# Performance work log

Hardware: AMD Instinct MI355X
Metric: run time of the kernel (lower is better)

## Reference

```python
import jax, jax.numpy as jnp
import numpy as np

EPS = 1e-8

def elu_feature_map(x):
    return jax.nn.elu(x) + 1.0

def setup_inputs() -> dict:
    key = jax.random.key(0)
    ks = jax.random.split(key, 5)
    B, S, D = 2, 4096, 1024
    scale = 1.0 / np.sqrt(D).astype(np.float32)
    x = jax.random.normal(ks[0], (B, S, D), dtype=jnp.float32)
    Wq = jax.random.normal(ks[1], (D, D), dtype=jnp.float32) * scale
    Wk = jax.random.normal(ks[2], (D, D), dtype=jnp.float32) * scale
    Wv = jax.random.normal(ks[3], (D, D), dtype=jnp.float32) * scale
    Wo = jax.random.normal(ks[4], (D, D), dtype=jnp.float32) * scale
    return {"x": x, "Wq": Wq, "Wk": Wk, "Wv": Wv, "Wo": Wo}

def reference(x, Wq, Wk, Wv, Wo):
    B, S, D = x.shape
    H = 16
    Dh = D // H
    # projections (nn.Linear with no bias: x @ W.T)
    def proj(W):
        return (x @ W.T).reshape(B, S, H, Dh)
    q = elu_feature_map(proj(Wq))  # [B,S,H,Dh]
    k = elu_feature_map(proj(Wk))
    v = proj(Wv)
    # scan over sequence: carry running kv_sum [B,H,Dh,Dh] and k_sum [B,H,Dh]
    q_t = jnp.moveaxis(q, 1, 0)  # [S,B,H,Dh]
    k_t = jnp.moveaxis(k, 1, 0)
    v_t = jnp.moveaxis(v, 1, 0)

    def step(carry, qkv):
        kv_sum, k_sum = carry
        q_i, k_i, v_i = qkv  # each [B,H,Dh]
        kv_sum = kv_sum + jnp.einsum('bhd,bhe->bhde', k_i, v_i)
        k_sum = k_sum + k_i
        num = jnp.einsum('bhd,bhde->bhe', q_i, kv_sum)
        den = jnp.sum(q_i * k_sum, axis=-1, keepdims=True)
        out_i = num / (den + EPS)
        return (kv_sum, k_sum), out_i

    kv0 = jnp.zeros((B, H, Dh, Dh), dtype=x.dtype)
    ks0 = jnp.zeros((B, H, Dh), dtype=x.dtype)
    _, out = jax.lax.scan(step, (kv0, ks0), (q_t, k_t, v_t))  # out: [S,B,H,Dh]
    out = jnp.moveaxis(out, 0, 1).reshape(B, S, D)
    return out @ Wo.T
```

## Files before the change

### kernel.cpp

```cpp
#include <hip/hip_runtime.h>
#include <math.h>


#define EPSF 1e-8f

typedef unsigned short u16;
typedef unsigned int   u32;
typedef __attribute__((ext_vector_type(8))) short short8v;
typedef __attribute__((ext_vector_type(4))) float f32x4;

__device__ __forceinline__ float elu1(float x){ return x > 0.f ? x + 1.f : __expf(x); }
__device__ __forceinline__ u16 f2bf(float f){
    union{float f; u32 i;} c; c.f = f;
    u32 i = c.i + 0x7FFFu + ((c.i >> 16) & 1u);
    return (u16)(i >> 16);
}
__device__ __forceinline__ float bflo(u32 v){ union{u32 i; float f;} c; c.i = v << 16; return c.f; }
__device__ __forceinline__ float bfhi(u32 v){ union{u32 i; float f;} c; c.i = v & 0xffff0000u; return c.f; }
__device__ __forceinline__ void f4a(float4 v, float* a){ a[0]=v.x; a[1]=v.y; a[2]=v.z; a[3]=v.w; }

__device__ __forceinline__ void gload16(const void* g, void* l){
    __builtin_amdgcn_global_load_lds((const __attribute__((address_space(1))) u32*)g,
                                     (__attribute__((address_space(3))) u32*)l, 16, 0, 0);
}

__global__ __launch_bounds__(256) void k_cast5(
    const float* __restrict__ x,  const float* __restrict__ wq,
    const float* __restrict__ wk, const float* __restrict__ wv,
    const float* __restrict__ wo,
    u16* __restrict__ xb, u16* __restrict__ wcat, u16* __restrict__ wob)
{
    size_t i8 = ((size_t)blockIdx.x * 256 + threadIdx.x) * 8;
    const float* s; u16* d; size_t off;
    if      (i8 <  8388608) { s = x;  d = xb;            off = i8; }
    else if (i8 <  9437184) { s = wq; d = wcat;          off = i8 - 8388608; }
    else if (i8 < 10485760) { s = wk; d = wcat + 1048576; off = i8 - 9437184; }
    else if (i8 < 11534336) { s = wv; d = wcat + 2097152; off = i8 - 10485760; }
    else                    { s = wo; d = wob;           off = i8 - 11534336; }
    float4 a = *(const float4*)&s[off];
    float4 b = *(const float4*)&s[off + 4];
    uint4 p;
    p.x = (u32)f2bf(a.x) | ((u32)f2bf(a.y) << 16);
    p.y = (u32)f2bf(a.z) | ((u32)f2bf(a.w) << 16);
    p.z = (u32)f2bf(b.x) | ((u32)f2bf(b.y) << 16);
    p.w = (u32)f2bf(b.z) | ((u32)f2bf(b.w) << 16);
    *(uint4*)&d[off] = p;
}

#define AOFF(BUF,KH) ((BUF)*49152 + (KH)*8192)
#define BOFF(BUF,KH) ((BUF)*49152 + 16384 + (KH)*16384)

#define ST(BUF, KT, KH) { \
    gload16(Ag + (size_t)(m0 + sRow)*1024 + (KT)*64 + (KH)*32 + sKg, dsm + AOFF(BUF,KH) + wvv*1024); \
    gload16(Wg + (size_t)(n0 + sRow)*1024 + (KT)*64 + (KH)*32 + sKg, dsm + BOFF(BUF,KH) + wvv*1024); \
    gload16(Wg + (size_t)(n0 + 128 + sRow)*1024 + (KT)*64 + (KH)*32 + sKg, dsm + BOFF(BUF,KH) + 8192 + wvv*1024); }

#define PH(BUF, KH, STCODE, CNT) { \
    short8v a[4], b[4]; \
    const char* Ab = dsm + AOFF(BUF,KH); \
    const char* Bb = dsm + BOFF(BUF,KH); \
    _Pragma("unroll") for (int m = 0; m < 4; ++m) a[m] = *(const short8v*)(Ab + offA[m]); \
    _Pragma("unroll") for (int n = 0; n < 4; ++n) b[n] = *(const short8v*)(Bb + offB[n]); \
    STCODE; \
    __builtin_amdgcn_s_setprio(1); \
    _Pragma("unroll") for (int m = 0; m < 4; ++m) \
        _Pragma("unroll") for (int n = 0; n < 4; ++n) \
            acc[m][n] = __builtin_amdgcn_mfma_f32_16x16x32_bf16(a[m], b[n], acc[m][n], 0, 0, 0); \
    __builtin_amdgcn_s_setprio(0); \
    asm volatile("s_waitcnt vmcnt(" #CNT ")" ::: "memory"); \
    __builtin_amdgcn_s_barrier(); }

template<int MODE, int NBY>
__global__ __launch_bounds__(512, 2) void k_gemm5(
    const u16* __restrict__ Ag, const u16* __restrict__ Wg, void* __restrict__ Cv)
{
    extern __shared__ char dsm[];
    const int nid = (blockIdx.x & 7) * ((64 * NBY) >> 3) + (blockIdx.x >> 3);
    const int bx  = nid / NBY;
    const int by  = nid % NBY;
    const int m0  = bx * 128;
    const int n0  = by * 256;

    const int tid = threadIdx.x;
    const int l   = tid & 63;
    const int wid = tid >> 6;
    const int wm  = wid >> 2;
    const int wn  = wid & 3;
    const int li  = l & 15;
    const int kgi = l >> 4;

    int offA[4], offB[4];
    #pragma unroll
    for (int m = 0; m < 4; ++m) {
        int ra = wm*64 + m*16 + li;
        offA[m] = (ra >> 1)*128 + (((((ra & 1) << 2) | kgi) ^ ((ra >> 1) & 7)) << 4);
        int rb = wn*64 + m*16 + li;
        offB[m] = (rb >> 1)*128 + (((((rb & 1) << 2) | kgi) ^ ((rb >> 1) & 7)) << 4);
    }
    const int wvv  = wid;
    const int sx   = (l & 7) ^ (l >> 3);
    const int sRow = 2*(wvv*8 + (l >> 3)) + (sx >> 2);
    const int sKg  = (sx & 3) * 8;

    f32x4 acc[4][4];
    #pragma unroll
    for (int m = 0; m < 4; ++m)
        #pragma unroll
        for (int n = 0; n < 4; ++n) acc[m][n] = (f32x4){0.f, 0.f, 0.f, 0.f};

    ST(0, 0, 0); ST(0, 0, 1); ST(1, 1, 0);
    asm volatile("s_waitcnt vmcnt(6)" ::: "memory");
    __builtin_amdgcn_s_barrier();

    #pragma unroll 1
    for (int it = 0; it < 7; ++it) {
        const int T = it * 2;
        PH(0, 0, ST(1, T+1, 1), 6);
        PH(0, 1, ST(0, T+2, 0), 6);
        PH(1, 0, ST(0, T+2, 1), 6);
        PH(1, 1, ST(1, T+3, 0), 6);
    }
    PH(0, 0, ST(1, 15, 1), 6);
    PH(0, 1, {}, 3);
    PH(1, 0, {}, 0);
    {
        short8v a[4], b[4];
        const char* Ab = dsm + AOFF(1,1);
        const char* Bb = dsm + BOFF(1,1);
        #pragma unroll
        for (int m = 0; m < 4; ++m) a[m] = *(const short8v*)(Ab + offA[m]);
        #pragma unroll
        for (int n = 0; n < 4; ++n) b[n] = *(const short8v*)(Bb + offB[n]);
        #pragma unroll
        for (int m = 0; m < 4; ++m)
            #pragma unroll
            for (int n = 0; n < 4; ++n)
                acc[m][n] = __builtin_amdgcn_mfma_f32_16x16x32_bf16(a[m], b[n], acc[m][n], 0, 0, 0);
    }

    const int r0 = m0 + wm*64 + (l >> 4) * 4;
    if (MODE == 1) {
        const int matrix = by >> 2;
        const bool do_elu = matrix < 2;
        u16* out = (u16*)Cv + (size_t)matrix * 8388608;
        const int c0 = (by & 3) * 256 + wn*64 + li;
        #pragma unroll
        for (int m = 0; m < 4; ++m)
            #pragma unroll
            for (int n = 0; n < 4; ++n)
                #pragma unroll
                for (int r = 0; r < 4; ++r) {
                    float v = acc[m][n][r];
                    if (do_elu) v = elu1(v);
                    out[(size_t)(r0 + m*16 + r) * 1024 + c0 + n*16] = f2bf(v);
                }
    } else {
        float* out = (float*)Cv;
        const int c0 = n0 + wn*64 + li;
        #pragma unroll
        for (int m = 0; m < 4; ++m)
            #pragma unroll
            for (int n = 0; n < 4; ++n)
                #pragma unroll
                for (int r = 0; r < 4; ++r)
                    out[(size_t)(r0 + m*16 + r) * 1024 + c0 + n*16] = acc[m][n][r];
    }
}

__global__ __launch_bounds__(256) void k_chunksums(
    const u16* __restrict__ Kg, const u16* __restrict__ Vg,
    float* __restrict__ CKVt, float* __restrict__ CKS)
{
    const int tid = threadIdx.x;
    const int tx = tid & 15, ty = tid >> 4;
    const int c  = blockIdx.x & 63;
    const int bh = blockIdx.x >> 6;
    const int b = bh >> 4, h = bh & 15;
    const int row0 = b * 4096 + c * 64;
    const int col  = h * 64;

    __shared__ float Ks[64][68];
    __shared__ float Vs[64][68];

    #pragma unroll
    for (int r = 0; r < 2; ++r) {
        int idx = tid + r * 256;
        int i = idx >> 3, cg = (idx & 7) << 3;
        uint4 ku = *(const uint4*)&Kg[(size_t)(row0 + i) * 1024 + col + cg];
        uint4 vu = *(const uint4*)&Vg[(size_t)(row0 + i) * 1024 + col + cg];
        Ks[i][cg+0]=bflo(ku.x); Ks[i][cg+1]=bfhi(ku.x);
        Ks[i][cg+2]=bflo(ku.y); Ks[i][cg+3]=bfhi(ku.y);
        Ks[i][cg+4]=bflo(ku.z); Ks[i][cg+5]=bfhi(ku.z);
        Ks[i][cg+6]=bflo(ku.w); Ks[i][cg+7]=bfhi(ku.w);
        Vs[i][cg+0]=bflo(vu.x); Vs[i][cg+1]=bfhi(vu.x);
        Vs[i][cg+2]=bflo(vu.y); Vs[i][cg+3]=bfhi(vu.y);
        Vs[i][cg+4]=bflo(vu.z); Vs[i][cg+5]=bfhi(vu.z);
        Vs[i][cg+6]=bflo(vu.w); Vs[i][cg+7]=bfhi(vu.w);
    }
    __syncthreads();

    float acc[4][4] = {};
    #pragma unroll 8
    for (int i = 0; i < 64; ++i) {
        float kv[4], vv[4];
        f4a(*(const float4*)&Ks[i][ty*4], kv);
        f4a(*(const float4*)&Vs[i][tx*4], vv);
        #pragma unroll
        for (int a = 0; a < 4; ++a)
            #pragma unroll
            for (int e = 0; e < 4; ++e)
                acc[a][e] = fmaf(kv[a], vv[e], acc[a][e]);
    }
    float* ckv = &CKVt[(size_t)blockIdx.x * 4096];
    #pragma unroll
    for (int e = 0; e < 4; ++e)
        *(float4*)&ckv[(tx*4 + e) * 64 + ty*4] =
            make_float4(acc[0][e], acc[1][e], acc[2][e], acc[3][e]);

    if (tid < 64) {
        float s = 0.f;
        #pragma unroll 8
        for (int i = 0; i < 64; ++i) s += Ks[i][tid];
        CKS[(size_t)blockIdx.x * 64 + tid] = s;
    }
}

__global__ __launch_bounds__(256) void k_prefix_kv(
    const float* __restrict__ CKVt, u16* __restrict__ CKVp)
{
    const int bh = blockIdx.x >> 4;
    const int p  = ((blockIdx.x & 15) << 8) + threadIdx.x;
    const size_t base = (size_t)bh * 64 * 4096 + p;
    float acc = 0.f;
    #pragma unroll
    for (int c = 0; c < 64; ++c) {
        float t = CKVt[base + (size_t)c * 4096];
        CKVp[base + (size_t)c * 4096] = f2bf(acc);
        acc += t;
    }
}

__global__ __launch_bounds__(256) void k_prefix_ks(float* __restrict__ CKS)
{
    const int idx = blockIdx.x * 256 + threadIdx.x;
    const int bh = idx >> 6, d = idx & 63;
    const size_t base = (size_t)bh * 64 * 64 + d;
    float v[64];
    #pragma unroll
    for (int c = 0; c < 64; ++c) v[c] = CKS[base + (size_t)c * 64];
    float acc = 0.f;
    #pragma unroll
    for (int c = 0; c < 64; ++c) { float t = v[c]; CKS[base + (size_t)c * 64] = acc; acc += t; }
}

#define LSTR 72
__global__ __launch_bounds__(256) void k_attn2(
    const u16* __restrict__ Qg, const u16* __restrict__ Kg, const u16* __restrict__ Vg,
    const u16* __restrict__ Stg, const float* __restrict__ KSg, u16* __restrict__ AO)
{
    const int tid = threadIdx.x;
    const int l = tid & 63;
    const int w = tid >> 6;
    const int c  = blockIdx.x & 63;
    const int bh = blockIdx.x >> 6;
    const int row0 = (bh >> 4) * 4096 + c * 64;
    const int col  = (bh & 15) * 64;

    __shared__ __align__(16) u16 Qs [64 * LSTR];
    __shared__ __align__(16) u16 Ks [64 * LSTR];
    __shared__ __align__(16) u16 Vt [64 * LSTR];
    __shared__ __align__(16) u16 Sts[64 * LSTR];
    __shared__ __align__(16) u16 Pl [64 * LSTR];
    __shared__ float ksumF[64];
    __shared__ float invdenL[64];

    #pragma unroll
    for (int r = 0; r < 2; ++r) {
        int idx = tid + r * 256;
        int i = idx >> 3, cg = (idx & 7) << 3;
        *(uint4*)&Qs [i*LSTR + cg] = *(const uint4*)&Qg [(size_t)(row0 + i) * 1024 + col + cg];
        *(uint4*)&Ks [i*LSTR + cg] = *(const uint4*)&Kg [(size_t)(row0 + i) * 1024 + col + cg];
        *(uint4*)&Sts[i*LSTR + cg] = *(const uint4*)&Stg[(size_t)blockIdx.x * 4096 + i * 64 + cg];
        uint4 vu = *(const uint4*)&Vg[(size_t)(row0 + i) * 1024 + col + cg];
        Vt[(cg+0)*LSTR + i] = (u16)(vu.x & 0xffff);
        Vt[(cg+1)*LSTR + i] = (u16)(vu.x >> 16);
        Vt[(cg+2)*LSTR + i] = (u16)(vu.y & 0xffff);
        Vt[(cg+3)*LSTR + i] = (u16)(vu.y >> 16);
        Vt[(cg+4)*LSTR + i] = (u16)(vu.z & 0xffff);
        Vt[(cg+5)*LSTR + i] = (u16)(vu.z >> 16);
        Vt[(cg+6)*LSTR + i] = (u16)(vu.w & 0xffff);
        Vt[(cg+7)*LSTR + i] = (u16)(vu.w >> 16);
    }
    if (tid < 64) ksumF[tid] = KSg[(size_t)blockIdx.x * 64 + tid];
    __syncthreads();

    const int li = l & 15;
    const int lg = l >> 4;
    const int i_row = w * 16 + li;

    short8v bq[2];
    #pragma unroll
    for (int kc = 0; kc < 2; ++kc)
        bq[kc] = *(const short8v*)&Qs[i_row * LSTR + lg*8 + kc*32];

    float den = EPSF;
    #pragma unroll
    for (int mj = 0; mj < 4; ++mj) {
        f32x4 sacc = (f32x4){0.f, 0.f, 0.f, 0.f};
        #pragma unroll
        for (int kc = 0; kc < 2; ++kc) {
            short8v ak = *(const short8v*)&Ks[(mj*16 + li) * LSTR + lg*8 + kc*32];
            sacc = __builtin_amdgcn_mfma_f32_16x16x32_bf16(ak, bq[kc], sacc, 0, 0, 0);
        }
        const int jbase = mj*16 + lg*4;
        float pv[4];
        #pragma unroll
        for (int r = 0; r < 4; ++r) {
            float v = sacc[r];
            v = (jbase + r <= i_row) ? v : 0.f;
            den += v;
            pv[r] = v;
        }
        u32 lo = (u32)f2bf(pv[0]) | ((u32)f2bf(pv[1]) << 16);
        u32 hi = (u32)f2bf(pv[2]) | ((u32)f2bf(pv[3]) << 16);
        *(uint2*)&Pl[i_row * LSTR + jbase] = make_uint2(lo, hi);
    }

    {
        const int d0 = lg * 16;
        uint4 q1 = *(const uint4*)&Qs[i_row * LSTR + d0];
        uint4 q2 = *(const uint4*)&Qs[i_row * LSTR + d0 + 8];
        den += bflo(q1.x)*ksumF[d0+0] + bfhi(q1.x)*ksumF[d0+1]
             + bflo(q1.y)*ksumF[d0+2] + bfhi(q1.y)*ksumF[d0+3]
             + bflo(q1.z)*ksumF[d0+4] + bfhi(q1.z)*ksumF[d0+5]
             + bflo(q1.w)*ksumF[d0+6] + bfhi(q1.w)*ksumF[d0+7]
             + bflo(q2.x)*ksumF[d0+8] + bfhi(q2.x)*ksumF[d0+9]
             + bflo(q2.y)*ksumF[d0+10]+ bfhi(q2.y)*ksumF[d0+11]
             + bflo(q2.z)*ksumF[d0+12]+ bfhi(q2.z)*ksumF[d0+13]
             + bflo(q2.w)*ksumF[d0+14]+ bfhi(q2.w)*ksumF[d0+15];
    }
    den += __shfl_xor(den, 16);
    den += __shfl_xor(den, 32);
    if (l < 16) invdenL[w*16 + l] = 1.f / den;

    f32x4 oacc[4];
    #pragma unroll
    for (int ne = 0; ne < 4; ++ne) oacc[ne] = (f32x4){0.f, 0.f, 0.f, 0.f};
    #pragma unroll
    for (int kc = 0; kc < 2; ++kc) {
        short8v ap = *(const short8v*)&Pl[i_row * LSTR + lg*8 + kc*32];
        short8v aq = bq[kc];
        #pragma unroll
        for (int ne = 0; ne < 4; ++ne) {
            short8v bv = *(const short8v*)&Vt [(ne*16 + li) * LSTR + lg*8 + kc*32];
            short8v bs = *(const short8v*)&Sts[(ne*16 + li) * LSTR + lg*8 + kc*32];
            oacc[ne] = __builtin_amdgcn_mfma_f32_16x16x32_bf16(ap, bv, oacc[ne], 0, 0, 0);
            oacc[ne] = __builtin_amdgcn_mfma_f32_16x16x32_bf16(aq, bs, oacc[ne], 0, 0, 0);
        }
    }

    float inv[4];
    #pragma unroll
    for (int r = 0; r < 4; ++r) inv[r] = invdenL[w*16 + lg*4 + r];
    #pragma unroll
    for (int ne = 0; ne < 4; ++ne)
        #pragma unroll
        for (int r = 0; r < 4; ++r)
            Pl[(w*16 + lg*4 + r) * LSTR + ne*16 + li] = f2bf(oacc[ne][r] * inv[r]);

    #pragma unroll
    for (int p = 0; p < 2; ++p) {
        int idx2 = l + p * 64;
        int ro = w*16 + (idx2 >> 3), cg = (idx2 & 7) << 3;
        *(uint4*)&AO[(size_t)(row0 + ro) * 1024 + col + cg] = *(const uint4*)&Pl[ro*LSTR + cg];
    }
}

extern "C" void kernel_launch(void* const* d_in, const int* in_sizes, int n_in,
                              void* d_out, int out_size, void* d_ws, size_t ws_size,
                              hipStream_t stream)
{
    const float* x  = (const float*)d_in[0];
    const float* Wq = (const float*)d_in[1];
    const float* Wk = (const float*)d_in[2];
    const float* Wv = (const float*)d_in[3];
    const float* Wo = (const float*)d_in[4];
    float* out = (float*)d_out;

    char* w = (char*)d_ws;
    u16*   QKVb = (u16*)(w);
    u16*   Qb   = QKVb;
    u16*   Kb   = QKVb + 8388608;
    u16*   Vb   = QKVb + 16777216;
    u16*   xb   = (u16*)(w + 50331648);
    u16*   AOb  = xb;
    u16*   Wcat = (u16*)(w + 67108864);
    u16*   Wob  = (u16*)(w + 73400320);
    float* CKV  = (float*)(w + 75497472);
    u16*   CKVp = (u16*)(w + 109051904);
    float* CKS  = (float*)(w + 125829120);

    hipFuncSetAttribute(reinterpret_cast<const void*>(k_gemm5<1,12>),
                        hipFuncAttributeMaxDynamicSharedMemorySize, 98304);
    hipFuncSetAttribute(reinterpret_cast<const void*>(k_gemm5<3,4>),
                        hipFuncAttributeMaxDynamicSharedMemorySize, 98304);

    k_cast5      <<<6144, 256, 0, stream>>>(x, Wq, Wk, Wv, Wo, xb, Wcat, Wob);
    k_gemm5<1,12><<<768,  512, 98304, stream>>>(xb, Wcat, (void*)QKVb);
    k_chunksums  <<<2048, 256, 0, stream>>>(Kb, Vb, CKV, CKS);
    k_prefix_kv  <<<512,  256, 0, stream>>>(CKV, CKVp);
    k_prefix_ks  <<<8,    256, 0, stream>>>(CKS);
    k_attn2      <<<2048, 256, 0, stream>>>(Qb, Kb, Vb, CKVp, CKS, AOb);
    k_gemm5<3,4> <<<256,  512, 98304, stream>>>(AOb, Wob, (void*)out);
}
```

Baseline: 142.6 us.

## Use new 256x128 tile QKV GEMM and store chunk KV sums in bf16 in place

Replaces the QKV projection GEMM with a new kernel that uses 256-thread blocks, a 256x128 output tile, a simpler double-buffered K loop, XOR-swizzled LDS and 48KB static shared memory so three blocks can share a CU. Separately, the per-chunk KV outer-product sums are now written as bf16 and prefix-summed in place, which halves that intermediate traffic and drops a buffer. The bf16 storage of the chunk sums before accumulation adds rounding error to the prefix, and the new GEMM's single-stage prefetch with a full wait each iteration may expose more memory latency.

```diff
diff --git a/kernel.cpp b/kernel.cpp
--- a/kernel.cpp
+++ b/kernel.cpp
@@ -15,6 +15,7 @@
     u32 i = c.i + 0x7FFFu + ((c.i >> 16) & 1u);
     return (u16)(i >> 16);
 }
+__device__ __forceinline__ float bf2f(u16 v){ union{u32 i; float f;} c; c.i = (u32)v << 16; return c.f; }
 __device__ __forceinline__ float bflo(u32 v){ union{u32 i; float f;} c; c.i = v << 16; return c.f; }
 __device__ __forceinline__ float bfhi(u32 v){ union{u32 i; float f;} c; c.i = v & 0xffff0000u; return c.f; }
 __device__ __forceinline__ void f4a(float4 v, float* a){ a[0]=v.x; a[1]=v.y; a[2]=v.z; a[3]=v.w; }
@@ -47,6 +48,94 @@
     *(uint4*)&d[off] = p;
 }
 
+__global__ __launch_bounds__(256, 3) void k_gemm6(
+    const u16* __restrict__ Ag, const u16* __restrict__ Wg, u16* __restrict__ C)
+{
+    __shared__ __align__(16) char dsm[49152];
+    const int bid = blockIdx.x;
+    const int nid = (bid & 7) * 96 + (bid >> 3);
+    const int bx  = nid / 24;
+    const int by  = nid % 24;
+    const int m0  = bx * 256;
+    const int n0  = by * 128;
+
+    const int tid = threadIdx.x;
+    const int l   = tid & 63;
+    const int wid = tid >> 6;
+    const int wm  = wid >> 1;
+    const int wn  = wid & 1;
+    const int li  = l & 15;
+    const int kgi = l >> 4;
+
+    const int ra0 = wm*128 + li;
+    const int offA0 = (ra0 >> 1)*128 + (((((ra0 & 1) << 2) | kgi) ^ ((ra0 >> 1) & 7)) << 4);
+    const int rb0 = wn*64 + li;
+    const int offB0 = (rb0 >> 1)*128 + (((((rb0 & 1) << 2) | kgi) ^ ((rb0 >> 1) & 7)) << 4);
+
+    const int sx   = (l & 7) ^ (l >> 3);
+    const int rowb = 2*(wid*8 + (l >> 3)) + (sx >> 2);
+    const int skg  = (sx & 3) * 8;
+    const u16* srcA = Ag + (size_t)(m0 + rowb) * 1024 + skg;
+    const u16* srcB = Wg + (size_t)(n0 + rowb) * 1024 + skg;
+
+    f32x4 acc[8][4];
+    #pragma unroll
+    for (int m = 0; m < 8; ++m)
+        #pragma unroll
+        for (int n = 0; n < 4; ++n) acc[m][n] = (f32x4){0.f, 0.f, 0.f, 0.f};
+
+    #define ST6(BUF, T) { \
+        char* ab = dsm + (BUF)*24576; \
+        char* bb = dsm + (BUF)*24576 + 16384; \
+        _Pragma("unroll") for (int j = 0; j < 4; ++j) \
+            gload16(srcA + (size_t)j*65536 + (T)*32, ab + j*4096 + wid*1024); \
+        _Pragma("unroll") for (int j = 0; j < 2; ++j) \
+            gload16(srcB + (size_t)j*65536 + (T)*32, bb + j*4096 + wid*1024); }
+
+    ST6(0, 0);
+    asm volatile("s_waitcnt vmcnt(0)" ::: "memory");
+    __builtin_amdgcn_s_barrier();
+
+    #pragma unroll 1
+    for (int t = 0; t < 32; ++t) {
+        const int cur = t & 1;
+        if (t < 31) ST6(cur ^ 1, t + 1);
+        const char* Ab = dsm + cur*24576;
+        const char* Bb = dsm + cur*24576 + 16384;
+        short8v bfr[4];
+        #pragma unroll
+        for (int n = 0; n < 4; ++n) bfr[n] = *(const short8v*)(Bb + offB0 + n*1024);
+        __builtin_amdgcn_s_setprio(1);
+        #pragma unroll
+        for (int m = 0; m < 8; ++m) {
+            short8v afr = *(const short8v*)(Ab + offA0 + m*1024);
+            #pragma unroll
+            for (int n = 0; n < 4; ++n)
+                acc[m][n] = __builtin_amdgcn_mfma_f32_16x16x32_bf16(afr, bfr[n], acc[m][n], 0, 0, 0);
+        }
+        __builtin_amdgcn_s_setprio(0);
+        asm volatile("s_waitcnt vmcnt(0)" ::: "memory");
+        __builtin_amdgcn_s_barrier();
+    }
+    #undef ST6
+
+    const int matrix = by >> 3;
+    const bool do_elu = matrix < 2;
+    u16* outp = C + (size_t)matrix * 8388608;
+    const int r0 = m0 + wm*128 + kgi*4;
+    const int c0 = (by & 7)*128 + wn*64 + li;
+    #pragma unroll
+    for (int m = 0; m < 8; ++m)
+        #pragma unroll
+        for (int n = 0; n < 4; ++n)
+            #pragma unroll
+            for (int r = 0; r < 4; ++r) {
+                float v = acc[m][n][r];
+                if (do_elu) v = elu1(v);
+                outp[(size_t)(r0 + m*16 + r) * 1024 + c0 + n*16] = f2bf(v);
+            }
+}
+
 #define AOFF(BUF,KH) ((BUF)*49152 + (KH)*8192)
 #define BOFF(BUF,KH) ((BUF)*49152 + 16384 + (KH)*16384)
 
@@ -70,9 +159,9 @@
     asm volatile("s_waitcnt vmcnt(" #CNT ")" ::: "memory"); \
     __builtin_amdgcn_s_barrier(); }
 
-template<int MODE, int NBY>
+template<int NBY>
 __global__ __launch_bounds__(512, 2) void k_gemm5(
-    const u16* __restrict__ Ag, const u16* __restrict__ Wg, void* __restrict__ Cv)
+    const u16* __restrict__ Ag, const u16* __restrict__ Wg, float* __restrict__ Cv)
 {
     extern __shared__ char dsm[];
     const int nid = (blockIdx.x & 7) * ((64 * NBY) >> 3) + (blockIdx.x >> 3);
@@ -139,37 +228,19 @@
     }
 
     const int r0 = m0 + wm*64 + (l >> 4) * 4;
-    if (MODE == 1) {
-        const int matrix = by >> 2;
-        const bool do_elu = matrix < 2;
-        u16* out = (u16*)Cv + (size_t)matrix * 8388608;
-        const int c0 = (by & 3) * 256 + wn*64 + li;
-        #pragma unroll
-        for (int m = 0; m < 4; ++m)
+    const int c0 = n0 + wn*64 + li;
+    #pragma unroll
+    for (int m = 0; m < 4; ++m)
+        #pragma unroll
+        for (int n = 0; n < 4; ++n)
             #pragma unroll
-            for (int n = 0; n < 4; ++n)
-                #pragma unroll
-                for (int r = 0; r < 4; ++r) {
-                    float v = acc[m][n][r];
-                    if (do_elu) v = elu1(v);
-                    out[(size_t)(r0 + m*16 + r) * 1024 + c0 + n*16] = f2bf(v);
-                }
-    } else {
-        float* out = (float*)Cv;
-        const int c0 = n0 + wn*64 + li;
-        #pragma unroll
-        for (int m = 0; m < 4; ++m)
-            #pragma unroll
-            for (int n = 0; n < 4; ++n)
-                #pragma unroll
-                for (int r = 0; r < 4; ++r)
-                    out[(size_t)(r0 + m*16 + r) * 1024 + c0 + n*16] = acc[m][n][r];
-    }
+            for (int r = 0; r < 4; ++r)
+                Cv[(size_t)(r0 + m*16 + r) * 1024 + c0 + n*16] = acc[m][n][r];
 }
 
 __global__ __launch_bounds__(256) void k_chunksums(
     const u16* __restrict__ Kg, const u16* __restrict__ Vg,
-    float* __restrict__ CKVt, float* __restrict__ CKS)
+    u16* __restrict__ CKVb, float* __restrict__ CKS)
 {
     const int tid = threadIdx.x;
     const int tx = tid & 15, ty = tid >> 4;
@@ -211,11 +282,13 @@
             for (int e = 0; e < 4; ++e)
                 acc[a][e] = fmaf(kv[a], vv[e], acc[a][e]);
     }
-    float* ckv = &CKVt[(size_t)blockIdx.x * 4096];
-    #pragma unroll
-    for (int e = 0; e < 4; ++e)
-        *(float4*)&ckv[(tx*4 + e) * 64 + ty*4] =
-            make_float4(acc[0][e], acc[1][e], acc[2][e], acc[3][e]);
+    u16* ckv = &CKVb[(size_t)blockIdx.x * 4096];
+    #pragma unroll
+    for (int e = 0; e < 4; ++e) {
+        u32 p0 = (u32)f2bf(acc[0][e]) | ((u32)f2bf(acc[1][e]) << 16);
+        u32 p1 = (u32)f2bf(acc[2][e]) | ((u32)f2bf(acc[3][e]) << 16);
+        *(uint2*)&ckv[(tx*4 + e) * 64 + ty*4] = make_uint2(p0, p1);
+    }
 
     if (tid < 64) {
         float s = 0.f;
@@ -225,8 +298,7 @@
     }
 }
 
-__global__ __launch_bounds__(256) void k_prefix_kv(
-    const float* __restrict__ CKVt, u16* __restrict__ CKVp)
+__global__ __launch_bounds__(256) void k_prefix_kv(u16* __restrict__ CKV)
 {
     const int bh = blockIdx.x >> 4;
     const int p  = ((blockIdx.x & 15) << 8) + threadIdx.x;
@@ -234,8 +306,8 @@
     float acc = 0.f;
     #pragma unroll
     for (int c = 0; c < 64; ++c) {
-        float t = CKVt[base + (size_t)c * 4096];
-        CKVp[base + (size_t)c * 4096] = f2bf(acc);
+        float t = bf2f(CKV[base + (size_t)c * 4096]);
+        CKV[base + (size_t)c * 4096] = f2bf(acc);
         acc += t;
     }
 }
@@ -396,20 +468,17 @@
     u16*   AOb  = xb;
     u16*   Wcat = (u16*)(w + 67108864);
     u16*   Wob  = (u16*)(w + 73400320);
-    float* CKV  = (float*)(w + 75497472);
-    u16*   CKVp = (u16*)(w + 109051904);
-    float* CKS  = (float*)(w + 125829120);
-
-    hipFuncSetAttribute(reinterpret_cast<const void*>(k_gemm5<1,12>),
+    u16*   CKVb = (u16*)(w + 75497472);
+    float* CKS  = (float*)(w + 92274688);
+
+    hipFuncSetAttribute(reinterpret_cast<const void*>(k_gemm5<4>),
                         hipFuncAttributeMaxDynamicSharedMemorySize, 98304);
-    hipFuncSetAttribute(reinterpret_cast<const void*>(k_gemm5<3,4>),
-                        hipFuncAttributeMaxDynamicSharedMemorySize, 98304);
-
-    k_cast5      <<<6144, 256, 0, stream>>>(x, Wq, Wk, Wv, Wo, xb, Wcat, Wob);
-    k_gemm5<1,12><<<768,  512, 98304, stream>>>(xb, Wcat, (void*)QKVb);
-    k_chunksums  <<<2048, 256, 0, stream>>>(Kb, Vb, CKV, CKS);
-    k_prefix_kv  <<<512,  256, 0, stream>>>(CKV, CKVp);
-    k_prefix_ks  <<<8,    256, 0, stream>>>(CKS);
-    k_attn2      <<<2048, 256, 0, stream>>>(Qb, Kb, Vb, CKVp, CKS, AOb);
-    k_gemm5<3,4> <<<256,  512, 98304, stream>>>(AOb, Wob, (void*)out);
-}
+
+    k_cast5    <<<6144, 256, 0, stream>>>(x, Wq, Wk, Wv, Wo, xb, Wcat, Wob);
+    k_gemm6    <<<768,  256, 0, stream>>>(xb, Wcat, QKVb);
+    k_chunksums<<<2048, 256, 0, stream>>>(Kb, Vb, CKVb, CKS);
+    k_prefix_kv<<<512,  256, 0, stream>>>(CKVb);
+    k_prefix_ks<<<8,    256, 0, stream>>>(CKS);
+    k_attn2    <<<2048, 256, 0, stream>>>(Qb, Kb, Vb, CKVb, CKS, AOb);
+    k_gemm5<4> <<<256,  512, 98304, stream>>>(AOb, Wob, out);
+}
```

After: 140.6 us. No clear change (-1.4%).
